# Performance work log

Hardware: AMD Instinct MI355X
Metric: run time of the kernel (lower is better)

## Reference

```python
import jax, jax.numpy as jnp
import numpy as np

N_NODES = 100000
N_EDGES = 1600000
VOCAB = 15000
D_IN = 128
D_HID = 128
N_GRAPHS = 16


def setup_inputs() -> dict:
    key = jax.random.key(0)
    ks = jax.random.split(key, 16)
    stdv = 1.0 / np.sqrt(D_HID)
    inp = {
        "word_ids": jax.random.randint(ks[0], (N_NODES,), 0, VOCAB),
        "edge_src": jax.random.randint(ks[1], (N_EDGES,), 0, N_NODES),
        "edge_dst": jax.random.randint(ks[2], (N_EDGES,), 0, N_NODES),
        "edge_weight": jax.random.uniform(ks[3], (N_EDGES,), dtype=jnp.float32),
        "norm": jax.random.uniform(ks[4], (N_NODES,), dtype=jnp.float32),
        "graph_id": jnp.sort(jax.random.randint(ks[5], (N_NODES,), 0, N_GRAPHS)),
        "y_data": jax.random.uniform(ks[6], (N_GRAPHS,), dtype=jnp.float32),
        # learned params
        "word_embeds": jax.random.normal(ks[7], (VOCAB, D_IN), dtype=jnp.float32) * 0.05,
        "W0": jax.random.uniform(ks[8], (D_IN, D_HID), minval=-stdv, maxval=stdv, dtype=jnp.float32),
        "b0": jax.random.uniform(ks[9], (D_HID,), minval=-stdv, maxval=stdv, dtype=jnp.float32),
        "W1": jax.random.uniform(ks[10], (D_HID, D_HID), minval=-stdv, maxval=stdv, dtype=jnp.float32),
        "b1": jax.random.uniform(ks[11], (D_HID,), minval=-stdv, maxval=stdv, dtype=jnp.float32),
        "Wout": jax.random.uniform(ks[12], (D_HID, 1), minval=-stdv, maxval=stdv, dtype=jnp.float32),
        "bout": jax.random.uniform(ks[13], (1,), minval=-stdv, maxval=stdv, dtype=jnp.float32),
    }
    return inp


def _gcn_layer(h, W, b, norm, edge_src, edge_dst, edge_weight):
    # h: [N, d_in] -> [N, d_out]
    h = h @ W                                   # dense projection
    h = h * norm[:, None]                       # pre-aggregation norm
    msg = h[edge_src] * edge_weight[:, None]    # u_mul_e   [E, d]
    h = jax.ops.segment_sum(msg, edge_dst, num_segments=N_NODES)  # sum agg
    h = h * norm[:, None]                       # post-aggregation norm
    return jax.nn.relu(h + b)


def reference(word_ids, edge_src, edge_dst, edge_weight, norm, graph_id, y_data,
              word_embeds, W0, b0, W1, b1, Wout, bout):
    h = word_embeds[word_ids]                   # [N, D_IN]
    h = _gcn_layer(h, W0, b0, norm, edge_src, edge_dst, edge_weight)
    h = _gcn_layer(h, W1, b1, norm, edge_src, edge_dst, edge_weight)
    # per-graph max pooling (dgl.max_nodes)
    g = jax.ops.segment_max(h, graph_id, num_segments=N_GRAPHS)   # [B, D_HID]
    z = g @ Wout + bout                          # [B, 1] logits
    zf = z.reshape(-1)
    # binary_cross_entropy_with_logits, mean reduction (numerically stable)
    loss = jnp.mean(jnp.maximum(zf, 0.0) - zf * y_data + jnp.log1p(jnp.exp(-jnp.abs(zf))))
    y_pred = jax.nn.sigmoid(z)
    return loss, y_pred
```

## Files before the change

### kernel.cpp

```cpp
#include <hip/hip_runtime.h>
#include <math.h>

#define D 128
#define NG 16
#define NBINS 512
#define CHUNK 2048
#define CAPB 4608

typedef unsigned int uint;
typedef unsigned short ushort;
typedef unsigned long long u64;
typedef __attribute__((ext_vector_type(8))) short bf16x8;
typedef __attribute__((ext_vector_type(4))) float f32x4;

__device__ __forceinline__ ushort f32_to_bf16(float f) {
    uint b = __float_as_uint(f);
    b += 0x7fffu + ((b >> 16) & 1u);
    return (ushort)(b >> 16);
}
__device__ __forceinline__ uint pack_bf16x2(float lo, float hi) {
    return (uint)f32_to_bf16(lo) | ((uint)f32_to_bf16(hi) << 16);
}
__device__ __forceinline__ float sb(uint u) {
    return (float)(int)(signed char)(u & 0xffu);
}

__global__ __launch_bounds__(256) void k_binA(
    const int* __restrict__ esrc, const int* __restrict__ edst,
    const float* __restrict__ ew, const float* __restrict__ norm,
    u64* __restrict__ binned, int* __restrict__ loc_off,
    int* __restrict__ bin_cnt, int ne, int width)
{
    __shared__ int hist[NBINS], lscan[NBINS], lcur[NBINS];
    __shared__ int ws4[4];
    __shared__ u64 stage[CHUNK];
    const int tid = threadIdx.x;
    const int base = blockIdx.x * CHUNK;
    const int count = min(CHUNK, ne - base);

    hist[tid] = 0; hist[tid + 256] = 0;
    __syncthreads();

    int s[8], bn[8], dl[8]; float c[8];
    #pragma unroll
    for (int i = 0; i < 8; ++i) {
        int li = i * 256 + tid;
        bn[i] = -1;
        if (li < count) {
            int e = base + li;
            s[i] = esrc[e];
            int d = edst[e];
            bn[i] = d / width;
            dl[i] = d - bn[i] * width;
            c[i] = ew[e] * norm[s[i]];
            atomicAdd(&hist[bn[i]], 1);
        }
    }
    __syncthreads();

    {
        int lane = tid & 63, w = tid >> 6;
        int h0 = hist[2 * tid], h1 = hist[2 * tid + 1];
        int sum = h0 + h1, x = sum;
        for (int dlt = 1; dlt < 64; dlt <<= 1) {
            int t2 = __shfl_up(x, dlt);
            if (lane >= dlt) x += t2;
        }
        if (lane == 63) ws4[w] = x;
        __syncthreads();
        if (tid == 0) { int run = 0; for (int i = 0; i < 4; ++i) { int t3 = ws4[i]; ws4[i] = run; run += t3; } }
        __syncthreads();
        int b0 = ws4[w] + (x - sum);
        lscan[2 * tid] = b0;       lscan[2 * tid + 1] = b0 + h0;
        lcur[2 * tid] = b0;        lcur[2 * tid + 1] = b0 + h0;
    }
    __syncthreads();

    int* lo = loc_off + (size_t)blockIdx.x * (NBINS + 1);
    lo[tid] = lscan[tid]; lo[tid + 256] = lscan[tid + 256];
    if (tid == 0) lo[NBINS] = count;
    if (hist[tid])       atomicAdd(&bin_cnt[tid], hist[tid]);
    if (hist[tid + 256]) atomicAdd(&bin_cnt[tid + 256], hist[tid + 256]);

    #pragma unroll
    for (int i = 0; i < 8; ++i) {
        if (bn[i] >= 0) {
            int pos = atomicAdd(&lcur[bn[i]], 1);
            uint packed = (uint)s[i] | ((uint)dl[i] << 24);
            stage[pos] = ((u64)__float_as_uint(c[i]) << 32) | packed;
        }
    }
    __syncthreads();

    u64* outp = binned + (size_t)blockIdx.x * CHUNK;
    for (int j = tid; j < count; j += 256) outp[j] = stage[j];
}

__global__ __launch_bounds__(1024) void k_scan_top(int* __restrict__ bsum, int nb)
{
    int tid = threadIdx.x, lane = tid & 63, w = tid >> 6;
    int v = tid < nb ? bsum[tid] : 0;
    int x = v;
    for (int d = 1; d < 64; d <<= 1) {
        int t = __shfl_up(x, d);
        if (lane >= d) x += t;
    }
    __shared__ int ws[16];
    if (lane == 63) ws[w] = x;
    __syncthreads();
    if (tid == 0) { int run = 0; for (int i = 0; i < 16; ++i) { int t = ws[i]; ws[i] = run; run += t; } }
    __syncthreads();
    x += ws[w];
    if (tid < nb) bsum[tid] = x - v;
}

__global__ __launch_bounds__(256) void k_binB(
    const u64* __restrict__ binned, const int* __restrict__ loc_off,
    const int* __restrict__ bin_off, int* __restrict__ off,
    int2* __restrict__ csr, int n, int ne, int width, int nA)
{
    __shared__ u64 stA[CAPB];
    __shared__ int hist[256], cur[256];
    __shared__ int wsum[4];
    __shared__ int sTotal;
    const int tid = threadIdx.x;
    const int bin = blockIdx.x;
    const int d0 = bin * width;
    const int dcount = min(n - d0, width);
    const int base = bin_off[bin];

    if (tid == 0) sTotal = 0;
    hist[tid] = 0;
    __syncthreads();

    if (dcount > 0) {
        for (int f = tid; f < nA; f += 256) {
            const int* lo = loc_off + (size_t)f * (NBINS + 1);
            int a = lo[bin], b = lo[bin + 1];
            int len = b - a;
            if (len > 0) {
                int st = atomicAdd(&sTotal, len);
                const u64* src = binned + (size_t)f * CHUNK + a;
                for (int k = 0; k < len; ++k) {
                    u64 r = src[k];
                    stA[st + k] = r;
                    atomicAdd(&hist[(int)((r >> 24) & 0xFF)], 1);
                }
            }
        }
    }
    __syncthreads();
    const int cnt = sTotal;

    {
        int lane = tid & 63, w = tid >> 6;
        int v = hist[tid], x = v;
        for (int dlt = 1; dlt < 64; dlt <<= 1) {
            int t2 = __shfl_up(x, dlt);
            if (lane >= dlt) x += t2;
        }
        if (lane == 63) wsum[w] = x;
        __syncthreads();
        if (tid == 0) { int run = 0; for (int i = 0; i < 4; ++i) { int t3 = wsum[i]; wsum[i] = run; run += t3; } }
        __syncthreads();
        int ex = wsum[w] + x - v;
        cur[tid] = ex;
        if (tid < dcount) off[d0 + tid] = base + ex;
    }
    if (tid == 0 && dcount > 0 && d0 + dcount == n) off[n] = base + cnt;
    __syncthreads();

    for (int i = tid; i < cnt; i += 256) {
        u64 r = stA[i];
        int dl = (int)((r >> 24) & 0xFF);
        int pos = atomicAdd(&cur[dl], 1);
        csr[base + pos] = make_int2((int)(r & 0xFFFFFF), (int)(r >> 32));
    }
}

__global__ __launch_bounds__(256) void k_cvt_bf16(
    const float* __restrict__ src, ushort* __restrict__ dst, int nelem)
{
    int i = (blockIdx.x * 256 + threadIdx.x) * 4;
    if (i + 3 < nelem) {
        float4 v = *reinterpret_cast<const float4*>(src + i);
        ushort4 o;
        o.x = f32_to_bf16(v.x); o.y = f32_to_bf16(v.y);
        o.z = f32_to_bf16(v.z); o.w = f32_to_bf16(v.w);
        *reinterpret_cast<ushort4*>(dst + i) = o;
    } else {
        for (int k = 0; k < 4 && i + k < nelem; ++k) dst[i + k] = f32_to_bf16(src[i + k]);
    }
}

__global__ __launch_bounds__(256) void k_wfrag(
    const float* __restrict__ W, ushort* __restrict__ Wf)
{
    int t = blockIdx.x * 256 + threadIdx.x;
    if (t >= 2048) return;
    int lane = t & 63, tile = t >> 6;
    int ks = tile & 3, nt = tile >> 2;
    int col = nt * 16 + (lane & 15);
    int k0 = ks * 32 + (lane >> 4) * 8;
    ushort* dst = Wf + (size_t)t * 8;
    #pragma unroll
    for (int j = 0; j < 8; ++j)
        dst[j] = f32_to_bf16(W[(k0 + j) * D + col]);
}

__global__ __launch_bounds__(256) void k_agg_bf16(
    const int* __restrict__ off, const int2* __restrict__ csr,
    const int* __restrict__ wid, const ushort* __restrict__ tab,
    ushort* __restrict__ outbf, int n)
{
    int row = blockIdx.x * 8 + (threadIdx.x >> 5);
    if (row >= n) return;
    int q = threadIdx.x & 31;
    int h = q >> 4;
    int c8 = (q & 15) * 8;
    int j0 = off[row], j1 = off[row + 1];
    float acc[8] = {0.f, 0.f, 0.f, 0.f, 0.f, 0.f, 0.f, 0.f};

    for (int jb = j0; jb < j1; jb += 32) {
        int m = min(32, j1 - jb);
        int2 p = make_int2(0, 0);
        if (q < m) {
            p = csr[jb + q];
            if (wid) p.x = wid[p.x];
        }
        int t = 0;
        for (; t + 8 <= m; t += 8) {
            uint4 u[4]; float wv[4];
            #pragma unroll
            for (int k = 0; k < 4; ++k) {
                int eh = t + 2 * k + h;
                int sv = __shfl(p.x, eh, 32);
                wv[k] = __int_as_float(__shfl(p.y, eh, 32));
                u[k] = *reinterpret_cast<const uint4*>(tab + (size_t)sv * D + c8);
            }
            #pragma unroll
            for (int k = 0; k < 4; ++k) {
                acc[0] = fmaf(__uint_as_float(u[k].x << 16),          wv[k], acc[0]);
                acc[1] = fmaf(__uint_as_float(u[k].x & 0xffff0000u),  wv[k], acc[1]);
                acc[2] = fmaf(__uint_as_float(u[k].y << 16),          wv[k], acc[2]);
                acc[3] = fmaf(__uint_as_float(u[k].y & 0xffff0000u),  wv[k], acc[3]);
                acc[4] = fmaf(__uint_as_float(u[k].z << 16),          wv[k], acc[4]);
                acc[5] = fmaf(__uint_as_float(u[k].z & 0xffff0000u),  wv[k], acc[5]);
                acc[6] = fmaf(__uint_as_float(u[k].w << 16),          wv[k], acc[6]);
                acc[7] = fmaf(__uint_as_float(u[k].w & 0xffff0000u),  wv[k], acc[7]);
            }
        }
        for (; t < m; t += 2) {
            int eh = t + h;
            int sv = __shfl(p.x, eh, 32);
            float wvv = __int_as_float(__shfl(p.y, eh, 32));
            uint4 u = *reinterpret_cast<const uint4*>(tab + (size_t)sv * D + c8);
            acc[0] = fmaf(__uint_as_float(u.x << 16),         wvv, acc[0]);
            acc[1] = fmaf(__uint_as_float(u.x & 0xffff0000u), wvv, acc[1]);
            acc[2] = fmaf(__uint_as_float(u.y << 16),         wvv, acc[2]);
            acc[3] = fmaf(__uint_as_float(u.y & 0xffff0000u), wvv, acc[3]);
            acc[4] = fmaf(__uint_as_float(u.z << 16),         wvv, acc[4]);
            acc[5] = fmaf(__uint_as_float(u.z & 0xffff0000u), wvv, acc[5]);
            acc[6] = fmaf(__uint_as_float(u.w << 16),         wvv, acc[6]);
            acc[7] = fmaf(__uint_as_float(u.w & 0xffff0000u), wvv, acc[7]);
        }
    }
    #pragma unroll
    for (int i = 0; i < 8; ++i) acc[i] += __shfl_xor(acc[i], 16, 32);
    if (h == 0) {
        uint4 o;
        o.x = pack_bf16x2(acc[0], acc[1]);
        o.y = pack_bf16x2(acc[2], acc[3]);
        o.z = pack_bf16x2(acc[4], acc[5]);
        o.w = pack_bf16x2(acc[6], acc[7]);
        *reinterpret_cast<uint4*>(outbf + (size_t)row * D + c8) = o;
    }
}

__global__ __launch_bounds__(256) void k_agg_q8(
    const int* __restrict__ off, const int2* __restrict__ csr,
    const char* __restrict__ tab8, const float* __restrict__ scale,
    ushort* __restrict__ outbf, int n)
{
    int row = blockIdx.x * 8 + (threadIdx.x >> 5);
    if (row >= n) return;
    int q = threadIdx.x & 31;
    int h = q >> 4;
    int c8 = (q & 15) * 8;
    int j0 = off[row], j1 = off[row + 1];
    float acc[8] = {0.f, 0.f, 0.f, 0.f, 0.f, 0.f, 0.f, 0.f};

    for (int jb = j0; jb < j1; jb += 32) {
        int m = min(32, j1 - jb);
        int2 p = make_int2(0, 0);
        if (q < m) p = csr[jb + q];
        int t = 0;
        for (; t + 8 <= m; t += 8) {
            uint2 u[4]; float wv[4];
            #pragma unroll
            for (int k = 0; k < 4; ++k) {
                int eh = t + 2 * k + h;
                int sv = __shfl(p.x, eh, 32);
                float wc = __int_as_float(__shfl(p.y, eh, 32));
                wv[k] = wc * scale[sv];
                u[k] = *reinterpret_cast<const uint2*>(tab8 + (size_t)sv * D + c8);
            }
            #pragma unroll
            for (int k = 0; k < 4; ++k) {
                acc[0] = fmaf(sb(u[k].x),       wv[k], acc[0]);
                acc[1] = fmaf(sb(u[k].x >> 8),  wv[k], acc[1]);
                acc[2] = fmaf(sb(u[k].x >> 16), wv[k], acc[2]);
                acc[3] = fmaf(sb(u[k].x >> 24), wv[k], acc[3]);
                acc[4] = fmaf(sb(u[k].y),       wv[k], acc[4]);
                acc[5] = fmaf(sb(u[k].y >> 8),  wv[k], acc[5]);
                acc[6] = fmaf(sb(u[k].y >> 16), wv[k], acc[6]);
                acc[7] = fmaf(sb(u[k].y >> 24), wv[k], acc[7]);
            }
        }
        for (; t < m; t += 2) {
            int eh = t + h;
            int sv = __shfl(p.x, eh, 32);
            float wc = __int_as_float(__shfl(p.y, eh, 32));
            float wvv = wc * scale[sv];
            uint2 u = *reinterpret_cast<const uint2*>(tab8 + (size_t)sv * D + c8);
            acc[0] = fmaf(sb(u.x),       wvv, acc[0]);
            acc[1] = fmaf(sb(u.x >> 8),  wvv, acc[1]);
            acc[2] = fmaf(sb(u.x >> 16), wvv, acc[2]);
            acc[3] = fmaf(sb(u.x >> 24), wvv, acc[3]);
            acc[4] = fmaf(sb(u.y),       wvv, acc[4]);
            acc[5] = fmaf(sb(u.y >> 8),  wvv, acc[5]);
            acc[6] = fmaf(sb(u.y >> 16), wvv, acc[6]);
            acc[7] = fmaf(sb(u.y >> 24), wvv, acc[7]);
        }
    }
    #pragma unroll
    for (int i = 0; i < 8; ++i) acc[i] += __shfl_xor(acc[i], 16, 32);
    if (h == 0) {
        uint4 o;
        o.x = pack_bf16x2(acc[0], acc[1]);
        o.y = pack_bf16x2(acc[2], acc[3]);
        o.z = pack_bf16x2(acc[4], acc[5]);
        o.w = pack_bf16x2(acc[6], acc[7]);
        *reinterpret_cast<uint4*>(outbf + (size_t)row * D + c8) = o;
    }
}

__device__ __forceinline__ void gemm_core_16x128(
    const ushort* __restrict__ aggbf, const ushort* __restrict__ Wf,
    int rowbase, int lane, int n, f32x4 acc[8])
{
    int arow = rowbase + (lane & 15);
    const bf16x8* WfV = reinterpret_cast<const bf16x8*>(Wf);
    #pragma unroll
    for (int ks = 0; ks < 4; ++ks) {
        bf16x8 af = {0, 0, 0, 0, 0, 0, 0, 0};
        if (arow < n) {
            int k0 = ks * 32 + (lane >> 4) * 8;
            af = *reinterpret_cast<const bf16x8*>(aggbf + (size_t)arow * D + k0);
        }
        #pragma unroll
        for (int nt = 0; nt < 8; ++nt) {
            bf16x8 bf = WfV[(nt * 4 + ks) * 64 + lane];
            acc[nt] = __builtin_amdgcn_mfma_f32_16x16x32_bf16(af, bf, acc[nt], 0, 0, 0);
        }
    }
}

__global__ __launch_bounds__(256) void k_gemm_mfma_post_q8(
    const ushort* __restrict__ aggbf, const ushort* __restrict__ Wf,
    const float* __restrict__ norm, const float* __restrict__ b,
    char* __restrict__ out8, float* __restrict__ scale, int n)
{
    int lane = threadIdx.x & 63;
    int w = threadIdx.x >> 6;
    int rowbase = blockIdx.x * 64 + w * 16;
    f32x4 acc[8] = {};
    gemm_core_16x128(aggbf, Wf, rowbase, lane, n, acc);

    int r0 = rowbase + (lane >> 4) * 4;
    float nrm[4];
    #pragma unroll
    for (int i = 0; i < 4; ++i) nrm[i] = (r0 + i < n) ? norm[r0 + i] : 0.f;

    float v[8][4];
    float mx[4] = {0.f, 0.f, 0.f, 0.f};
    #pragma unroll
    for (int nt = 0; nt < 8; ++nt) {
        float bc = b[nt * 16 + (lane & 15)];
        #pragma unroll
        for (int i = 0; i < 4; ++i) {
            float t = fmaxf(fmaf(acc[nt][i], nrm[i], bc), 0.f);
            v[nt][i] = t;
            mx[i] = fmaxf(mx[i], t);
        }
    }
    #pragma unroll
    for (int d = 1; d < 16; d <<= 1) {
        #pragma unroll
        for (int i = 0; i < 4; ++i) mx[i] = fmaxf(mx[i], __shfl_xor(mx[i], d, 64));
    }
    float inv[4];
    #pragma unroll
    for (int i = 0; i < 4; ++i) inv[i] = (mx[i] > 0.f) ? 127.f / mx[i] : 0.f;
    if ((lane & 15) == 0) {
        #pragma unroll
        for (int i = 0; i < 4; ++i)
            if (r0 + i < n) scale[r0 + i] = (mx[i] > 0.f) ? mx[i] * (1.f / 127.f) : 0.f;
    }
    #pragma unroll
    for (int nt = 0; nt < 8; ++nt) {
        int col = nt * 16 + (lane & 15);
        #pragma unroll
        for (int i = 0; i < 4; ++i) {
            int r = r0 + i;
            if (r < n) {
                int qv = __float2int_rn(v[nt][i] * inv[i]);
                out8[(size_t)r * D + col] = (char)min(qv, 127);
            }
        }
    }
}

__global__ __launch_bounds__(256) void k_gemm_mfma_segmax(
    const ushort* __restrict__ aggbf, const ushort* __restrict__ Wf,
    const float* __restrict__ norm, const float* __restrict__ b,
    const int* __restrict__ gid, unsigned* __restrict__ g, int n)
{
    __shared__ float sh[64][132];
    __shared__ int sgid[64];
    int lane = threadIdx.x & 63;
    int w = threadIdx.x >> 6;
    int rowbase = blockIdx.x * 64 + w * 16;
    f32x4 acc[8] = {};
    gemm_core_16x128(aggbf, Wf, rowbase, lane, n, acc);

    int r0 = rowbase + (lane >> 4) * 4;
    int lr0 = w * 16 + (lane >> 4) * 4;
    float nrm[4];
    #pragma unroll
    for (int i = 0; i < 4; ++i) nrm[i] = (r0 + i < n) ? norm[r0 + i] : 0.f;
    #pragma unroll
    for (int nt = 0; nt < 8; ++nt) {
        int col = nt * 16 + (lane & 15);
        float bc = b[col];
        #pragma unroll
        for (int i = 0; i < 4; ++i) {
            float v = (r0 + i < n) ? fmaxf(fmaf(acc[nt][i], nrm[i], bc), 0.f) : 0.f;
            sh[lr0 + i][col] = v;
        }
    }
    if (threadIdx.x < 64) {
        int r = blockIdx.x * 64 + threadIdx.x;
        sgid[threadIdx.x] = (r < n) ? gid[r] : -1;
    }
    __syncthreads();

    if (threadIdx.x < D) {
        int c = threadIdx.x;
        int glo = 0x7fffffff, ghi = -1;
        #pragma unroll
        for (int i = 0; i < 64; ++i) {
            int gv = sgid[i];
            if (gv >= 0) { glo = min(glo, gv); ghi = max(ghi, gv); }
        }
        for (int gr = glo; gr <= ghi; ++gr) {
            float m = 0.f;
            #pragma unroll
            for (int i = 0; i < 64; ++i)
                if (sgid[i] == gr) m = fmaxf(m, sh[i][c]);
            if (m > 0.f) atomicMax(&g[gr * D + c], __float_as_uint(m));
        }
    }
}

__global__ __launch_bounds__(1024) void k_final(
    const unsigned* __restrict__ g, const float* __restrict__ Wout,
    const float* __restrict__ bout, const float* __restrict__ y,
    float* __restrict__ out)
{
    __shared__ float zs[NG];
    int wave = threadIdx.x >> 6, lane = threadIdx.x & 63;
    float acc = 0.f;
    for (int c = lane; c < D; c += 64)
        acc += __uint_as_float(g[wave * D + c]) * Wout[c];
    for (int off2 = 32; off2; off2 >>= 1) acc += __shfl_down(acc, off2);
    if (lane == 0) {
        float z = acc + bout[0];
        zs[wave] = z;
        out[1 + wave] = 1.f / (1.f + expf(-z));
    }
    __syncthreads();
    if (threadIdx.x == 0) {
        float loss = 0.f;
        for (int i = 0; i < NG; ++i) {
            float z = zs[i];
            loss += fmaxf(z, 0.f) - z * y[i] + log1pf(expf(-fabsf(z)));
        }
        out[0] = loss / NG;
    }
}

extern "C" void kernel_launch(void* const* d_in, const int* in_sizes, int n_in,
                              void* d_out, int out_size, void* d_ws, size_t ws_size,
                              hipStream_t stream) {
    const int*   word_ids = (const int*)  d_in[0];
    const int*   esrc     = (const int*)  d_in[1];
    const int*   edst     = (const int*)  d_in[2];
    const float* ew       = (const float*)d_in[3];
    const float* norm     = (const float*)d_in[4];
    const int*   gid      = (const int*)  d_in[5];
    const float* y        = (const float*)d_in[6];
    const float* embeds   = (const float*)d_in[7];
    const float* W0       = (const float*)d_in[8];
    const float* b0       = (const float*)d_in[9];
    const float* W1       = (const float*)d_in[10];
    const float* b1       = (const float*)d_in[11];
    const float* Wout     = (const float*)d_in[12];
    const float* bout     = (const float*)d_in[13];

    const int n  = in_sizes[0];
    const int ne = in_sizes[1];
    const int vocab = in_sizes[7] / D;
    float* out = (float*)d_out;

    const int nA = (ne + CHUNK - 1) / CHUNK;
    const int width = (n + NBINS - 1) / NBINS;

    ushort* aggbf = (ushort*)d_ws;
    int*    off   = (int*)(aggbf + (size_t)n * D);
    int*    bcnt  = off + (n + 1);
    int*    loff  = bcnt + NBINS;
    uintptr_t bin_addr = ((uintptr_t)(loff + (size_t)nA * (NBINS + 1)) + 15) & ~(uintptr_t)15;
    u64*    binned = (u64*)bin_addr;
    int2*   csr   = (int2*)(binned + (size_t)nA * CHUNK);
    char*   h1q   = (char*)(csr + ne);
    float*  hscale = (float*)(h1q + (size_t)n * D);
    ushort* emb16 = (ushort*)(hscale + n);
    unsigned* g   = (unsigned*)(emb16 + (size_t)vocab * D);
    uintptr_t wf_addr = ((uintptr_t)(g + NG * D) + 15) & ~(uintptr_t)15;
    ushort* w0f = (ushort*)wf_addr;
    ushort* w1f = w0f + D * D;

    const dim3 blk(256);
    const int ablocks = (n + 7) / 8;
    const int mblocks = (n + 63) / 64;

    hipMemsetAsync(bcnt, 0, NBINS * sizeof(int), stream);
    k_binA<<<nA, blk, 0, stream>>>(esrc, edst, ew, norm, binned, loff, bcnt, ne, width);
    k_scan_top<<<1, 1024, 0, stream>>>(bcnt, NBINS);
    k_binB<<<NBINS, blk, 0, stream>>>(binned, loff, bcnt, off, csr, n, ne, width, nA);

    k_cvt_bf16<<<(vocab * D / 4 + 255) / 256, blk, 0, stream>>>(embeds, emb16, vocab * D);
    k_wfrag<<<8, blk, 0, stream>>>(W0, w0f);
    k_wfrag<<<8, blk, 0, stream>>>(W1, w1f);

    k_agg_bf16<<<ablocks, blk, 0, stream>>>(off, csr, word_ids, emb16, aggbf, n);
    k_gemm_mfma_post_q8<<<mblocks, blk, 0, stream>>>(aggbf, w0f, norm, b0, h1q, hscale, n);

    k_agg_q8<<<ablocks, blk, 0, stream>>>(off, csr, h1q, hscale, aggbf, n);
    hipMemsetAsync(g, 0, NG * D * sizeof(unsigned), stream);
    k_gemm_mfma_segmax<<<mblocks, blk, 0, stream>>>(aggbf, w1f, norm, b1, gid, g, n);

    k_final<<<1, 1024, 0, stream>>>(g, Wout, bout, y, out);
}
```

Before: 226.8 us.

## Project vocab embeddings before aggregation and fuse layer-0 epilogue into gather

Uses linearity to apply W0 to the 15k-row embedding table up front, giving a projected table P, instead of projecting the 100k aggregated node rows. The layer-0 aggregation then gathers from P and applies the norm, bias, ReLU and int8 quantisation in the same kernel. This removes the separate bf16 conversion kernel, the 100k-row GEMM and the bf16 intermediate round trip. Rounding changes a little because P is stored as bf16 before aggregation.

```diff
diff --git a/kernel.cpp b/kernel.cpp
--- a/kernel.cpp
+++ b/kernel.cpp
@@ -178,21 +178,6 @@
     }
 }
 
-__global__ __launch_bounds__(256) void k_cvt_bf16(
-    const float* __restrict__ src, ushort* __restrict__ dst, int nelem)
-{
-    int i = (blockIdx.x * 256 + threadIdx.x) * 4;
-    if (i + 3 < nelem) {
-        float4 v = *reinterpret_cast<const float4*>(src + i);
-        ushort4 o;
-        o.x = f32_to_bf16(v.x); o.y = f32_to_bf16(v.y);
-        o.z = f32_to_bf16(v.z); o.w = f32_to_bf16(v.w);
-        *reinterpret_cast<ushort4*>(dst + i) = o;
-    } else {
-        for (int k = 0; k < 4 && i + k < nelem; ++k) dst[i + k] = f32_to_bf16(src[i + k]);
-    }
-}
-
 __global__ __launch_bounds__(256) void k_wfrag(
     const float* __restrict__ W, ushort* __restrict__ Wf)
 {
@@ -208,10 +193,51 @@
         dst[j] = f32_to_bf16(W[(k0 + j) * D + col]);
 }
 
-__global__ __launch_bounds__(256) void k_agg_bf16(
+__global__ __launch_bounds__(256) void k_proj(
+    const float* __restrict__ emb, const ushort* __restrict__ Wf,
+    ushort* __restrict__ P, int vocab)
+{
+    int lane = threadIdx.x & 63;
+    int w = threadIdx.x >> 6;
+    int rowbase = blockIdx.x * 64 + w * 16;
+    int arow = rowbase + (lane & 15);
+    const bf16x8* WfV = reinterpret_cast<const bf16x8*>(Wf);
+    f32x4 acc[8] = {};
+    #pragma unroll
+    for (int ks = 0; ks < 4; ++ks) {
+        bf16x8 af = {0, 0, 0, 0, 0, 0, 0, 0};
+        if (arow < vocab) {
+            int k0 = ks * 32 + (lane >> 4) * 8;
+            float4 a0 = *reinterpret_cast<const float4*>(emb + (size_t)arow * D + k0);
+            float4 a1 = *reinterpret_cast<const float4*>(emb + (size_t)arow * D + k0 + 4);
+            af[0] = (short)f32_to_bf16(a0.x); af[1] = (short)f32_to_bf16(a0.y);
+            af[2] = (short)f32_to_bf16(a0.z); af[3] = (short)f32_to_bf16(a0.w);
+            af[4] = (short)f32_to_bf16(a1.x); af[5] = (short)f32_to_bf16(a1.y);
+            af[6] = (short)f32_to_bf16(a1.z); af[7] = (short)f32_to_bf16(a1.w);
+        }
+        #pragma unroll
+        for (int nt = 0; nt < 8; ++nt) {
+            bf16x8 bf = WfV[(nt * 4 + ks) * 64 + lane];
+            acc[nt] = __builtin_amdgcn_mfma_f32_16x16x32_bf16(af, bf, acc[nt], 0, 0, 0);
+        }
+    }
+    int r0 = rowbase + (lane >> 4) * 4;
+    #pragma unroll
+    for (int nt = 0; nt < 8; ++nt) {
+        int col = nt * 16 + (lane & 15);
+        #pragma unroll
+        for (int i = 0; i < 4; ++i) {
+            int r = r0 + i;
+            if (r < vocab) P[(size_t)r * D + col] = f32_to_bf16(acc[nt][i]);
+        }
+    }
+}
+
+__global__ __launch_bounds__(256) void k_agg_proj(
     const int* __restrict__ off, const int2* __restrict__ csr,
-    const int* __restrict__ wid, const ushort* __restrict__ tab,
-    ushort* __restrict__ outbf, int n)
+    const int* __restrict__ wid, const ushort* __restrict__ P,
+    const float* __restrict__ norm, const float* __restrict__ bias,
+    char* __restrict__ out8, float* __restrict__ scale, int n)
 {
     int row = blockIdx.x * 8 + (threadIdx.x >> 5);
     if (row >= n) return;
@@ -226,7 +252,7 @@
         int2 p = make_int2(0, 0);
         if (q < m) {
             p = csr[jb + q];
-            if (wid) p.x = wid[p.x];
+            p.x = wid[p.x];
         }
         int t = 0;
         for (; t + 8 <= m; t += 8) {
@@ -236,7 +262,7 @@
                 int eh = t + 2 * k + h;
                 int sv = __shfl(p.x, eh, 32);
                 wv[k] = __int_as_float(__shfl(p.y, eh, 32));
-                u[k] = *reinterpret_cast<const uint4*>(tab + (size_t)sv * D + c8);
+                u[k] = *reinterpret_cast<const uint4*>(P + (size_t)sv * D + c8);
             }
             #pragma unroll
             for (int k = 0; k < 4; ++k) {
@@ -254,7 +280,7 @@
             int eh = t + h;
             int sv = __shfl(p.x, eh, 32);
             float wvv = __int_as_float(__shfl(p.y, eh, 32));
-            uint4 u = *reinterpret_cast<const uint4*>(tab + (size_t)sv * D + c8);
+            uint4 u = *reinterpret_cast<const uint4*>(P + (size_t)sv * D + c8);
             acc[0] = fmaf(__uint_as_float(u.x << 16),         wvv, acc[0]);
             acc[1] = fmaf(__uint_as_float(u.x & 0xffff0000u), wvv, acc[1]);
             acc[2] = fmaf(__uint_as_float(u.y << 16),         wvv, acc[2]);
@@ -267,13 +293,40 @@
     }
     #pragma unroll
     for (int i = 0; i < 8; ++i) acc[i] += __shfl_xor(acc[i], 16, 32);
+
+    float nm = norm[row];
+    float4 bv0 = *reinterpret_cast<const float4*>(bias + c8);
+    float4 bv1 = *reinterpret_cast<const float4*>(bias + c8 + 4);
+    float v[8];
+    v[0] = fmaxf(fmaf(acc[0], nm, bv0.x), 0.f);
+    v[1] = fmaxf(fmaf(acc[1], nm, bv0.y), 0.f);
+    v[2] = fmaxf(fmaf(acc[2], nm, bv0.z), 0.f);
+    v[3] = fmaxf(fmaf(acc[3], nm, bv0.w), 0.f);
+    v[4] = fmaxf(fmaf(acc[4], nm, bv1.x), 0.f);
+    v[5] = fmaxf(fmaf(acc[5], nm, bv1.y), 0.f);
+    v[6] = fmaxf(fmaf(acc[6], nm, bv1.z), 0.f);
+    v[7] = fmaxf(fmaf(acc[7], nm, bv1.w), 0.f);
+    float mx = v[0];
+    #pragma unroll
+    for (int i = 1; i < 8; ++i) mx = fmaxf(mx, v[i]);
+    #pragma unroll
+    for (int d = 1; d < 16; d <<= 1) mx = fmaxf(mx, __shfl_xor(mx, d, 32));
+
+    float inv = (mx > 0.f) ? 127.f / mx : 0.f;
+    if (q == 0) scale[row] = (mx > 0.f) ? mx * (1.f / 127.f) : 0.f;
     if (h == 0) {
-        uint4 o;
-        o.x = pack_bf16x2(acc[0], acc[1]);
-        o.y = pack_bf16x2(acc[2], acc[3]);
-        o.z = pack_bf16x2(acc[4], acc[5]);
-        o.w = pack_bf16x2(acc[6], acc[7]);
-        *reinterpret_cast<uint4*>(outbf + (size_t)row * D + c8) = o;
+        uint b0 = 0, b1 = 0;
+        #pragma unroll
+        for (int i = 0; i < 4; ++i) {
+            int qv = min(__float2int_rn(v[i] * inv), 127);
+            b0 |= ((uint)qv & 0xffu) << (8 * i);
+        }
+        #pragma unroll
+        for (int i = 0; i < 4; ++i) {
+            int qv = min(__float2int_rn(v[4 + i] * inv), 127);
+            b1 |= ((uint)qv & 0xffu) << (8 * i);
+        }
+        *reinterpret_cast<uint2*>(out8 + (size_t)row * D + c8) = make_uint2(b0, b1);
     }
 }
 
@@ -366,61 +419,6 @@
     }
 }
 
-__global__ __launch_bounds__(256) void k_gemm_mfma_post_q8(
-    const ushort* __restrict__ aggbf, const ushort* __restrict__ Wf,
-    const float* __restrict__ norm, const float* __restrict__ b,
-    char* __restrict__ out8, float* __restrict__ scale, int n)
-{
-    int lane = threadIdx.x & 63;
-    int w = threadIdx.x >> 6;
-    int rowbase = blockIdx.x * 64 + w * 16;
-    f32x4 acc[8] = {};
-    gemm_core_16x128(aggbf, Wf, rowbase, lane, n, acc);
-
-    int r0 = rowbase + (lane >> 4) * 4;
-    float nrm[4];
-    #pragma unroll
-    for (int i = 0; i < 4; ++i) nrm[i] = (r0 + i < n) ? norm[r0 + i] : 0.f;
-
-    float v[8][4];
-    float mx[4] = {0.f, 0.f, 0.f, 0.f};
-    #pragma unroll
-    for (int nt = 0; nt < 8; ++nt) {
-        float bc = b[nt * 16 + (lane & 15)];
-        #pragma unroll
-        for (int i = 0; i < 4; ++i) {
-            float t = fmaxf(fmaf(acc[nt][i], nrm[i], bc), 0.f);
-            v[nt][i] = t;
-            mx[i] = fmaxf(mx[i], t);
-        }
-    }
-    #pragma unroll
-    for (int d = 1; d < 16; d <<= 1) {
-        #pragma unroll
-        for (int i = 0; i < 4; ++i) mx[i] = fmaxf(mx[i], __shfl_xor(mx[i], d, 64));
-    }
-    float inv[4];
-    #pragma unroll
-    for (int i = 0; i < 4; ++i) inv[i] = (mx[i] > 0.f) ? 127.f / mx[i] : 0.f;
-    if ((lane & 15) == 0) {
-        #pragma unroll
-        for (int i = 0; i < 4; ++i)
-            if (r0 + i < n) scale[r0 + i] = (mx[i] > 0.f) ? mx[i] * (1.f / 127.f) : 0.f;
-    }
-    #pragma unroll
-    for (int nt = 0; nt < 8; ++nt) {
-        int col = nt * 16 + (lane & 15);
-        #pragma unroll
-        for (int i = 0; i < 4; ++i) {
-            int r = r0 + i;
-            if (r < n) {
-                int qv = __float2int_rn(v[nt][i] * inv[i]);
-                out8[(size_t)r * D + col] = (char)min(qv, 127);
-            }
-        }
-    }
-}
-
 __global__ __launch_bounds__(256) void k_gemm_mfma_segmax(
     const ushort* __restrict__ aggbf, const ushort* __restrict__ Wf,
     const float* __restrict__ norm, const float* __restrict__ b,
@@ -535,8 +533,9 @@
     int2*   csr   = (int2*)(binned + (size_t)nA * CHUNK);
     char*   h1q   = (char*)(csr + ne);
     float*  hscale = (float*)(h1q + (size_t)n * D);
-    ushort* emb16 = (ushort*)(hscale + n);
-    unsigned* g   = (unsigned*)(emb16 + (size_t)vocab * D);
+    uintptr_t p_addr = ((uintptr_t)(hscale + n) + 15) & ~(uintptr_t)15;
+    ushort* P     = (ushort*)p_addr;
+    unsigned* g   = (unsigned*)(P + (size_t)vocab * D);
     uintptr_t wf_addr = ((uintptr_t)(g + NG * D) + 15) & ~(uintptr_t)15;
     ushort* w0f = (ushort*)wf_addr;
     ushort* w1f = w0f + D * D;
@@ -544,18 +543,18 @@
     const dim3 blk(256);
     const int ablocks = (n + 7) / 8;
     const int mblocks = (n + 63) / 64;
+    const int pblocks = (vocab + 63) / 64;
 
     hipMemsetAsync(bcnt, 0, NBINS * sizeof(int), stream);
     k_binA<<<nA, blk, 0, stream>>>(esrc, edst, ew, norm, binned, loff, bcnt, ne, width);
     k_scan_top<<<1, 1024, 0, stream>>>(bcnt, NBINS);
     k_binB<<<NBINS, blk, 0, stream>>>(binned, loff, bcnt, off, csr, n, ne, width, nA);
 
-    k_cvt_bf16<<<(vocab * D / 4 + 255) / 256, blk, 0, stream>>>(embeds, emb16, vocab * D);
     k_wfrag<<<8, blk, 0, stream>>>(W0, w0f);
     k_wfrag<<<8, blk, 0, stream>>>(W1, w1f);
-
-    k_agg_bf16<<<ablocks, blk, 0, stream>>>(off, csr, word_ids, emb16, aggbf, n);
-    k_gemm_mfma_post_q8<<<mblocks, blk, 0, stream>>>(aggbf, w0f, norm, b0, h1q, hscale, n);
+    k_proj<<<pblocks, blk, 0, stream>>>(embeds, w0f, P, vocab);
+
+    k_agg_proj<<<ablocks, blk, 0, stream>>>(off, csr, word_ids, P, norm, b0, h1q, hscale, n);
 
     k_agg_q8<<<ablocks, blk, 0, stream>>>(off, csr, h1q, hscale, aggbf, n);
     hipMemsetAsync(g, 0, NG * D * sizeof(unsigned), stream);
```

Measured after the change: 216.0 us. -4.8%, faster.
